# Kernel optimization log

Hardware: AMD Instinct MI355X
Metric: run time of the kernel (lower is better)

## Reference

```python
import jax, jax.numpy as jnp
import numpy as np

CHUNK = 128  # intra-chunk causal block size for the chunked linear-attention scan


def setup_inputs() -> dict:
    key = jax.random.key(0)
    ks = jax.random.split(key, 7)
    B, H, N, D, F = 1, 24, 4096, 128, 256
    q = jax.random.normal(ks[0], (B, H, N, D), dtype=jnp.float32)
    k = jax.random.normal(ks[1], (B, H, N, D), dtype=jnp.float32)
    v = jax.random.normal(ks[2], (B, H, N, D), dtype=jnp.float32)
    # fan-in scaling so phi features / accumulated state stay numerically sane
    w1 = jax.random.normal(ks[3], (F, D), dtype=jnp.float32) * (D ** -0.5)
    b1 = jax.random.normal(ks[4], (F,), dtype=jnp.float32) * 0.02
    w2 = jax.random.normal(ks[5], (F, F), dtype=jnp.float32) * (F ** -0.5)
    b2 = jax.random.normal(ks[6], (F,), dtype=jnp.float32) * 0.02
    return {"q": q, "k": k, "v": v, "w1": w1, "b1": b1, "w2": w2, "b2": b2}


def _phi(x, w1, b1, w2, b2):
    # Linear(D->F) -> SiLU -> Linear(F->F)
    h = jax.nn.silu(jnp.einsum('bnd,fd->bnf', x, w1) + b1)
    return jnp.einsum('bnf,gf->bng', h, w2) + b2


def _causal_scan(qp, kp, vf):
    # out_t = q_t . (sum_{s<=t} k_s v_s^T) / (t+1), chunked parallel form.
    BH, N, F = qp.shape
    D = vf.shape[-1]
    C = CHUNK
    nC = N // C
    qc = qp.reshape(BH, nC, C, F).transpose(1, 0, 2, 3)  # [nC,BH,C,F]
    kc = kp.reshape(BH, nC, C, F).transpose(1, 0, 2, 3)
    vc = vf.reshape(BH, nC, C, D).transpose(1, 0, 2, 3)
    offsets = (jnp.arange(nC) * C).astype(qp.dtype)
    mask = jnp.tril(jnp.ones((C, C), dtype=qp.dtype))  # include diagonal
    pos = jnp.arange(1, C + 1, dtype=qp.dtype)

    def step(w, inp):
        qb, kb, vb, off = inp
        inter = jnp.einsum('bcf,bfd->bcd', qb, w)
        attn = jnp.einsum('bcf,bsf->bcs', qb, kb) * mask
        intra = jnp.einsum('bcs,bsd->bcd', attn, vb)
        counts = off + pos  # global (token_idx + 1)
        out = (inter + intra) / counts[None, :, None]
        w = w + jnp.einsum('bcf,bcd->bfd', kb, vb)
        return w, out

    w0 = jnp.zeros((BH, F, D), dtype=qp.dtype)
    _, outs = jax.lax.scan(step, w0, (qc, kc, vc, offsets))  # outs [nC,BH,C,D]
    return outs.transpose(1, 0, 2, 3).reshape(BH, N, D)


def reference(q, k, v, w1, b1, w2, b2):
    B, H, N, D = q.shape
    qf = q.reshape(B * H, N, D)
    kf = k.reshape(B * H, N, D)
    vf = v.reshape(B * H, N, D)
    qp = _phi(qf, w1, b1, w2, b2)
    kp = _phi(kf, w1, b1, w2, b2)
    out_fwd = _causal_scan(qp, kp, vf)
    out_rev = _causal_scan(qp[:, ::-1], kp[:, ::-1], vf[:, ::-1])[:, ::-1]
    return (out_fwd + out_rev).reshape(B, H, N, D)
```

## Files before the change

### kernel.cpp

```cpp
#include <hip/hip_runtime.h>


typedef __attribute__((ext_vector_type(8))) _Float16 f16x8;
typedef __attribute__((ext_vector_type(4))) _Float16 f16x4;
typedef __attribute__((ext_vector_type(4))) float f32x4;

#define MFMA16(a, b, c) __builtin_amdgcn_mfma_f32_16x16x32_f16((a), (b), (c), 0, 0, 0)

constexpr int BH   = 24;
constexpr int NSEQ = 4096;
constexpr int DD   = 128;
constexpr int FF   = 256;
constexpr int CHK  = 128;
constexpr int NC   = NSEQ / CHK;
constexpr int NROWS = BH * NSEQ;

__global__ void prep_kernel(const float* __restrict__ w1, const float* __restrict__ w2,
                            _Float16* __restrict__ w1h, _Float16* __restrict__ w2h) {
  int i = blockIdx.x * 256 + threadIdx.x;
  if (i < FF * DD) w1h[i] = (_Float16)w1[i];
  if (i < FF * FF) w2h[i] = (_Float16)w2[i];
}

__global__ void vt_kernel(const float* __restrict__ v, _Float16* __restrict__ vT) {
  __shared__ __align__(16) _Float16 lt[128][136];
  int blk = blockIdx.x;
  int c = blk & 31, bh = blk >> 5;
  const float* vc = v + ((size_t)bh * NSEQ + c * CHK) * DD;
  int tid = threadIdx.x;
#pragma unroll
  for (int it = 0; it < 16; ++it) {
    int flat = it * 1024 + tid * 4;
    int s = flat >> 7, d0 = flat & 127;
    float4 xv = *(const float4*)&vc[(size_t)s * DD + d0];
    lt[d0 + 0][s] = (_Float16)xv.x;
    lt[d0 + 1][s] = (_Float16)xv.y;
    lt[d0 + 2][s] = (_Float16)xv.z;
    lt[d0 + 3][s] = (_Float16)xv.w;
  }
  __syncthreads();
#pragma unroll
  for (int it = 0; it < 8; ++it) {
    int flat = it * 256 + tid;
    int d = flat >> 4, sg = flat & 15;
    *(f16x8*)&vT[((size_t)bh * DD + d) * NSEQ + c * CHK + sg * 8] =
        *(const f16x8*)&lt[d][sg * 8];
  }
}

__global__ __launch_bounds__(512, 2)
void phi_kernel(const float* __restrict__ q, const float* __restrict__ k,
                const float* __restrict__ b1, const float* __restrict__ b2,
                const _Float16* __restrict__ w1h, const _Float16* __restrict__ w2h,
                _Float16* __restrict__ qp, _Float16* __restrict__ kp,
                _Float16* __restrict__ kpT) {
  __shared__ __align__(16) char smem[137216];
  _Float16 (*xs)[136]  = (_Float16(*)[136])smem;
  _Float16 (*w1s)[136] = (_Float16(*)[136])(smem + 34816);
  _Float16 (*hs)[264]  = (_Float16(*)[264])smem;
  _Float16 (*w2s)[136] = (_Float16(*)[136])(smem + 67584);
  int blk = blockIdx.x;
  const float* src;
  _Float16* dst;
  bool isk;
  int rb;
  if (blk < NROWS / 128) { src = q; dst = qp; rb = blk * 128; isk = false; }
  else                   { src = k; dst = kp; rb = (blk - NROWS / 128) * 128; isk = true; }
  int tid = threadIdx.x;
  int lane = tid & 63, wv = tid >> 6, lr = lane & 15, lq = lane >> 4;

#pragma unroll
  for (int it = 0; it < 8; ++it) {
    int flat = it * 512 + tid;
    int f = flat >> 4, cg = flat & 15;
    *(f16x8*)&w1s[f][cg * 8] = *(const f16x8*)&w1h[f * DD + cg * 8];
  }
#pragma unroll
  for (int it = 0; it < 8; ++it) {
    int flat = it * 512 + tid;
    int r = flat >> 5, dg = flat & 31;
    float4 xv = *(const float4*)&src[(size_t)(rb + r) * DD + dg * 4];
    f16x4 hv = {(_Float16)xv.x, (_Float16)xv.y, (_Float16)xv.z, (_Float16)xv.w};
    *(f16x4*)&xs[r][dg * 4] = hv;
  }
  __syncthreads();

  int wm1 = wv & 1, wn1 = wv >> 1;
  f32x4 acc[4][4] = {};
#pragma unroll
  for (int ks = 0; ks < 4; ++ks) {
    f16x8 av[4];
#pragma unroll
    for (int im = 0; im < 4; ++im)
      av[im] = *(const f16x8*)&xs[wm1 * 64 + im * 16 + lr][ks * 32 + lq * 8];
#pragma unroll
    for (int fn = 0; fn < 4; ++fn) {
      f16x8 bv = *(const f16x8*)&w1s[wn1 * 64 + fn * 16 + lr][ks * 32 + lq * 8];
#pragma unroll
      for (int im = 0; im < 4; ++im) acc[im][fn] = MFMA16(av[im], bv, acc[im][fn]);
    }
  }
  __syncthreads();

#pragma unroll
  for (int it = 0; it < 8; ++it) {
    int flat = it * 512 + tid;
    int g = flat >> 4, cg = flat & 15;
    *(f16x8*)&w2s[g][cg * 8] = *(const f16x8*)&w2h[(size_t)g * FF + cg * 8];
  }
#pragma unroll
  for (int im = 0; im < 4; ++im)
#pragma unroll
    for (int fn = 0; fn < 4; ++fn) {
      int f = wn1 * 64 + fn * 16 + lr;
      float bb = b1[f];
      int r0 = wm1 * 64 + im * 16 + lq * 4;
#pragma unroll
      for (int r = 0; r < 4; ++r) {
        float xv = acc[im][fn][r] + bb;
        hs[r0 + r][f] = (_Float16)(xv / (1.0f + __expf(-xv)));
      }
    }
  __syncthreads();

  int wmg = wv & 1, wng = wv >> 1;
  f32x4 ac2[4][4] = {};
#pragma unroll
  for (int ks = 0; ks < 4; ++ks) {
    f16x8 av[4];
#pragma unroll
    for (int im = 0; im < 4; ++im)
      av[im] = *(const f16x8*)&hs[wmg * 64 + im * 16 + lr][ks * 32 + lq * 8];
#pragma unroll
    for (int fn = 0; fn < 4; ++fn) {
      f16x8 bv = *(const f16x8*)&w2s[wng * 64 + fn * 16 + lr][ks * 32 + lq * 8];
#pragma unroll
      for (int im = 0; im < 4; ++im) ac2[im][fn] = MFMA16(av[im], bv, ac2[im][fn]);
    }
  }
  __syncthreads();
#pragma unroll
  for (int it = 0; it < 8; ++it) {
    int flat = it * 512 + tid;
    int g = flat >> 4, cg = flat & 15;
    *(f16x8*)&w2s[g][cg * 8] = *(const f16x8*)&w2h[(size_t)g * FF + 128 + cg * 8];
  }
  __syncthreads();
#pragma unroll
  for (int ks = 0; ks < 4; ++ks) {
    f16x8 av[4];
#pragma unroll
    for (int im = 0; im < 4; ++im)
      av[im] = *(const f16x8*)&hs[wmg * 64 + im * 16 + lr][128 + ks * 32 + lq * 8];
#pragma unroll
    for (int fn = 0; fn < 4; ++fn) {
      f16x8 bv = *(const f16x8*)&w2s[wng * 64 + fn * 16 + lr][ks * 32 + lq * 8];
#pragma unroll
      for (int im = 0; im < 4; ++im) ac2[im][fn] = MFMA16(av[im], bv, ac2[im][fn]);
    }
  }

  int bh = rb >> 12, s0 = rb & 4095;
#pragma unroll
  for (int im = 0; im < 4; ++im)
#pragma unroll
    for (int fn = 0; fn < 4; ++fn) {
      int g = wng * 64 + fn * 16 + lr;
      float bb = b2[g];
      int r0 = wmg * 64 + im * 16 + lq * 4;
#pragma unroll
      for (int r = 0; r < 4; ++r) {
        _Float16 val = (_Float16)(ac2[im][fn][r] + bb);
        dst[(size_t)(rb + r0 + r) * FF + g] = val;
        if (isk) kpT[((size_t)bh * FF + g) * NSEQ + s0 + r0 + r] = val;
      }
    }
}

__global__ __launch_bounds__(512, 2)
void s_kernel(const _Float16* __restrict__ vT, const _Float16* __restrict__ kpT,
              _Float16* __restrict__ S) {
  __shared__ __align__(16) _Float16 vt[128][136];
  __shared__ __align__(16) _Float16 kt[256][136];
  int blk = blockIdx.x;
  int c = blk & 31, bh = blk >> 5;
  int tid = threadIdx.x;
#pragma unroll
  for (int it = 0; it < 4; ++it) {
    int flat = it * 512 + tid;
    int d = flat >> 4, sg = flat & 15;
    *(f16x8*)&vt[d][sg * 8] = *(const f16x8*)&vT[((size_t)bh * DD + d) * NSEQ + c * CHK + sg * 8];
  }
#pragma unroll
  for (int it = 0; it < 8; ++it) {
    int flat = it * 512 + tid;
    int f = flat >> 4, sg = flat & 15;
    *(f16x8*)&kt[f][sg * 8] = *(const f16x8*)&kpT[((size_t)bh * FF + f) * NSEQ + c * CHK + sg * 8];
  }
  __syncthreads();
  int lane = tid & 63, wv = tid >> 6, lr = lane & 15, lq = lane >> 4;
  int wmd = wv & 1, wnf = wv >> 1;
  f32x4 acc[4][4] = {};
#pragma unroll
  for (int ks = 0; ks < 4; ++ks) {
    f16x8 av[4];
#pragma unroll
    for (int im = 0; im < 4; ++im)
      av[im] = *(const f16x8*)&vt[wmd * 64 + im * 16 + lr][ks * 32 + lq * 8];
#pragma unroll
    for (int fn = 0; fn < 4; ++fn) {
      f16x8 bv = *(const f16x8*)&kt[wnf * 64 + fn * 16 + lr][ks * 32 + lq * 8];
#pragma unroll
      for (int im = 0; im < 4; ++im) acc[im][fn] = MFMA16(av[im], bv, acc[im][fn]);
    }
  }
  _Float16* Sp = S + ((size_t)bh * NC + c) * (size_t)(DD * FF);
#pragma unroll
  for (int im = 0; im < 4; ++im)
#pragma unroll
    for (int fn = 0; fn < 4; ++fn) {
      int f = wnf * 64 + fn * 16 + lr;
#pragma unroll
      for (int r = 0; r < 4; ++r) {
        int d = wmd * 64 + im * 16 + lq * 4 + r;
        Sp[(size_t)d * FF + f] = (_Float16)acc[im][fn][r];
      }
    }
}

__global__ void prefix_kernel(_Float16* S_Wr, _Float16* __restrict__ Wf) {
  size_t idx = (size_t)blockIdx.x * 256 + threadIdx.x;
  int bh = (int)(idx >> 15);
  int df = (int)(idx & 32767);
  size_t base = (size_t)bh * NC * 32768 + df;
  float vals[NC];
#pragma unroll
  for (int c = 0; c < NC; ++c) vals[c] = (float)S_Wr[base + (size_t)c * 32768];
  float run = 0.f;
#pragma unroll
  for (int c = 0; c < NC; ++c) { Wf[base + (size_t)c * 32768] = (_Float16)run; run += vals[c]; }
  run = 0.f;
#pragma unroll
  for (int c = NC - 1; c >= 0; --c) { S_Wr[base + (size_t)c * 32768] = (_Float16)run; run += vals[c]; }
}

__global__ __launch_bounds__(512, 2)
void scan_kernel(const _Float16* __restrict__ qp, const _Float16* __restrict__ kp,
                 const _Float16* __restrict__ vT, const _Float16* __restrict__ Wf,
                 const _Float16* __restrict__ Wr, float* __restrict__ out) {
  __shared__ __align__(16) _Float16 vt[128][136];
  __shared__ __align__(16) _Float16 P[128][136];
  int blk = blockIdx.x;
  int c = blk & 31, bh = blk >> 5;
  const _Float16* qpc = qp + ((size_t)bh * NSEQ + c * CHK) * FF;
  const _Float16* kpc = kp + ((size_t)bh * NSEQ + c * CHK) * FF;
  int tid = threadIdx.x, lane = tid & 63, wv = tid >> 6, lr = lane & 15, lq = lane >> 4;
  int wm = wv & 3, wn = wv >> 2;

  f16x8 aq[2][8];
#pragma unroll
  for (int im = 0; im < 2; ++im)
#pragma unroll
    for (int ks = 0; ks < 8; ++ks)
      aq[im][ks] = *(const f16x8*)&qpc[(size_t)(wm * 32 + im * 16 + lr) * FF + ks * 32 + lq * 8];
#pragma unroll
  for (int it = 0; it < 4; ++it) {
    int flat = it * 512 + tid;
    int d = flat >> 4, sg = flat & 15;
    *(f16x8*)&vt[d][sg * 8] = *(const f16x8*)&vT[((size_t)bh * DD + d) * NSEQ + c * CHK + sg * 8];
  }
  f16x8 bk[2][8];
#pragma unroll
  for (int ks = 0; ks < 8; ++ks)
    bk[0][ks] = *(const f16x8*)&kpc[(size_t)(wn * 64 + lr) * FF + ks * 32 + lq * 8];
  f32x4 pacc[2][4] = {};
#pragma unroll
  for (int j = 0; j < 4; ++j) {
    int cur = j & 1;
    if (j < 3)
#pragma unroll
      for (int ks = 0; ks < 8; ++ks)
        bk[cur ^ 1][ks] = *(const f16x8*)&kpc[(size_t)(wn * 64 + (j + 1) * 16 + lr) * FF + ks * 32 + lq * 8];
#pragma unroll
    for (int ks = 0; ks < 8; ++ks)
#pragma unroll
      for (int im = 0; im < 2; ++im)
        pacc[im][j] = MFMA16(aq[im][ks], bk[cur][ks], pacc[im][j]);
  }
#pragma unroll
  for (int im = 0; im < 2; ++im)
#pragma unroll
    for (int j = 0; j < 4; ++j)
#pragma unroll
      for (int r = 0; r < 4; ++r)
        P[wm * 32 + im * 16 + lq * 4 + r][wn * 64 + j * 16 + lr] = (_Float16)pacc[im][j][r];

  const _Float16* Wfc = Wf + ((size_t)bh * NC + c) * (size_t)(DD * FF);
  const _Float16* Wrc = Wr + ((size_t)bh * NC + c) * (size_t)(DD * FF);
  f16x8 bf[8], br[8];
#pragma unroll
  for (int ks = 0; ks < 8; ++ks) {
    int d = wn * 64 + lr;
    bf[ks] = *(const f16x8*)&Wfc[(size_t)d * FF + ks * 32 + lq * 8];
    br[ks] = *(const f16x8*)&Wrc[(size_t)d * FF + ks * 32 + lq * 8];
  }
  __syncthreads();

  f32x4 af[2][4] = {}, ar[2][4] = {};
#pragma unroll
  for (int jd = 0; jd < 4; ++jd) {
#pragma unroll
    for (int ks = 0; ks < 8; ++ks)
#pragma unroll
      for (int im = 0; im < 2; ++im) {
        af[im][jd] = MFMA16(aq[im][ks], bf[ks], af[im][jd]);
        ar[im][jd] = MFMA16(aq[im][ks], br[ks], ar[im][jd]);
      }
    if (jd < 3)
#pragma unroll
      for (int ks = 0; ks < 8; ++ks) {
        int d = wn * 64 + (jd + 1) * 16 + lr;
        bf[ks] = *(const f16x8*)&Wfc[(size_t)d * FF + ks * 32 + lq * 8];
        br[ks] = *(const f16x8*)&Wrc[(size_t)d * FF + ks * 32 + lq * 8];
      }
    {
      int ks = jd;
      f16x8 bv[4];
#pragma unroll
      for (int jd2 = 0; jd2 < 4; ++jd2)
        bv[jd2] = *(const f16x8*)&vt[wn * 64 + jd2 * 16 + lr][ks * 32 + lq * 8];
#pragma unroll
      for (int im = 0; im < 2; ++im) {
        int irow = wm * 32 + im * 16 + lr;
        f16x8 p = *(const f16x8*)&P[irow][ks * 32 + lq * 8];
        f16x8 pf = p, pr = p;
#pragma unroll
        for (int jj = 0; jj < 8; ++jj) {
          int s = ks * 32 + lq * 8 + jj;
          pf[jj] = (s <= irow) ? p[jj] : (_Float16)0.0f;
          pr[jj] = (s >= irow) ? p[jj] : (_Float16)0.0f;
        }
#pragma unroll
        for (int jd2 = 0; jd2 < 4; ++jd2) {
          af[im][jd2] = MFMA16(pf, bv[jd2], af[im][jd2]);
          ar[im][jd2] = MFMA16(pr, bv[jd2], ar[im][jd2]);
        }
      }
    }
  }

  float* oc = out + ((size_t)bh * NSEQ + c * CHK) * DD;
#pragma unroll
  for (int im = 0; im < 2; ++im)
#pragma unroll
    for (int jd = 0; jd < 4; ++jd) {
      int d = wn * 64 + jd * 16 + lr;
#pragma unroll
      for (int r = 0; r < 4; ++r) {
        int il = wm * 32 + im * 16 + lq * 4 + r;
        int gi = c * CHK + il;
        oc[(size_t)il * DD + d] = af[im][jd][r] / (float)(gi + 1) + ar[im][jd][r] / (float)(NSEQ - gi);
      }
    }
}

extern "C" void kernel_launch(void* const* d_in, const int* in_sizes, int n_in,
                              void* d_out, int out_size, void* d_ws, size_t ws_size,
                              hipStream_t stream) {
  const float* q  = (const float*)d_in[0];
  const float* k  = (const float*)d_in[1];
  const float* v  = (const float*)d_in[2];
  const float* w1 = (const float*)d_in[3];
  const float* b1 = (const float*)d_in[4];
  const float* w2 = (const float*)d_in[5];
  const float* b2 = (const float*)d_in[6];
  float* out = (float*)d_out;

  char* ws = (char*)d_ws;
  const size_t SZ = 50331648ull;
  _Float16* w1h = (_Float16*)(ws);
  _Float16* w2h = (_Float16*)(ws + 65536);
  _Float16* qp  = (_Float16*)(ws + 196608);
  _Float16* kp  = (_Float16*)(ws + 196608 + SZ);
  _Float16* kpT = (_Float16*)(ws + 196608 + 2 * SZ);
  _Float16* S   = (_Float16*)(ws + 196608 + 3 * SZ);
  _Float16* vT  = (_Float16*)(ws + 196608 + 4 * SZ);
  _Float16* Wf  = kpT;
  _Float16* Wr  = S;

  prep_kernel<<<dim3(256), dim3(256), 0, stream>>>(w1, w2, w1h, w2h);
  vt_kernel<<<dim3(BH * NC), dim3(256), 0, stream>>>(v, vT);
  phi_kernel<<<dim3(2 * NROWS / 128), dim3(512), 0, stream>>>(q, k, b1, b2, w1h, w2h, qp, kp, kpT);
  s_kernel<<<dim3(BH * NC), dim3(512), 0, stream>>>(vT, kpT, S);
  prefix_kernel<<<dim3(BH * DD * FF / 256), dim3(256), 0, stream>>>(S, Wf);
  scan_kernel<<<dim3(BH * NC), dim3(512), 0, stream>>>(qp, kp, vT, Wf, Wr, out);
}
```

Baseline: 416.0 us.

## Shrink phi and S tiles for occupancy, keep weights in registers, vectorize prefix scan

```diff
diff --git a/kernel.cpp b/kernel.cpp
--- a/kernel.cpp
+++ b/kernel.cpp
@@ -48,126 +48,106 @@
   }
 }
 
-__global__ __launch_bounds__(512, 2)
+__global__ __launch_bounds__(512, 4)
 void phi_kernel(const float* __restrict__ q, const float* __restrict__ k,
                 const float* __restrict__ b1, const float* __restrict__ b2,
                 const _Float16* __restrict__ w1h, const _Float16* __restrict__ w2h,
                 _Float16* __restrict__ qp, _Float16* __restrict__ kp,
                 _Float16* __restrict__ kpT) {
-  __shared__ __align__(16) char smem[137216];
-  _Float16 (*xs)[136]  = (_Float16(*)[136])smem;
-  _Float16 (*w1s)[136] = (_Float16(*)[136])(smem + 34816);
-  _Float16 (*hs)[264]  = (_Float16(*)[264])smem;
-  _Float16 (*w2s)[136] = (_Float16(*)[136])(smem + 67584);
+  __shared__ __align__(16) _Float16 xs[64][136];
+  __shared__ __align__(16) _Float16 hs[64][264];
   int blk = blockIdx.x;
   const float* src;
   _Float16* dst;
   bool isk;
   int rb;
-  if (blk < NROWS / 128) { src = q; dst = qp; rb = blk * 128; isk = false; }
-  else                   { src = k; dst = kp; rb = (blk - NROWS / 128) * 128; isk = true; }
+  if (blk < NROWS / 64) { src = q; dst = qp; rb = blk * 64; isk = false; }
+  else                  { src = k; dst = kp; rb = (blk - NROWS / 64) * 64; isk = true; }
   int tid = threadIdx.x;
   int lane = tid & 63, wv = tid >> 6, lr = lane & 15, lq = lane >> 4;
-
-#pragma unroll
-  for (int it = 0; it < 8; ++it) {
-    int flat = it * 512 + tid;
-    int f = flat >> 4, cg = flat & 15;
-    *(f16x8*)&w1s[f][cg * 8] = *(const f16x8*)&w1h[f * DD + cg * 8];
-  }
-#pragma unroll
-  for (int it = 0; it < 8; ++it) {
-    int flat = it * 512 + tid;
-    int r = flat >> 5, dg = flat & 31;
-    float4 xv = *(const float4*)&src[(size_t)(rb + r) * DD + dg * 4];
+  int wn = wv;
+
+  f16x8 w1r[4][2];
+#pragma unroll
+  for (int ks = 0; ks < 4; ++ks)
+#pragma unroll
+    for (int fn = 0; fn < 2; ++fn)
+      w1r[ks][fn] = *(const f16x8*)&w1h[(wn * 32 + fn * 16 + lr) * DD + ks * 32 + lq * 8];
+
+#pragma unroll
+  for (int it = 0; it < 4; ++it) {
+    int flat = it * 2048 + tid * 4;
+    int r = flat >> 7, c = flat & 127;
+    float4 xv = *(const float4*)&src[(size_t)(rb + r) * DD + c];
     f16x4 hv = {(_Float16)xv.x, (_Float16)xv.y, (_Float16)xv.z, (_Float16)xv.w};
-    *(f16x4*)&xs[r][dg * 4] = hv;
-  }
-  __syncthreads();
-
-  int wm1 = wv & 1, wn1 = wv >> 1;
-  f32x4 acc[4][4] = {};
+    *(f16x4*)&xs[r][c] = hv;
+  }
+  __syncthreads();
+
+  f32x4 acc[4][2] = {};
 #pragma unroll
   for (int ks = 0; ks < 4; ++ks) {
     f16x8 av[4];
 #pragma unroll
     for (int im = 0; im < 4; ++im)
-      av[im] = *(const f16x8*)&xs[wm1 * 64 + im * 16 + lr][ks * 32 + lq * 8];
-#pragma unroll
-    for (int fn = 0; fn < 4; ++fn) {
-      f16x8 bv = *(const f16x8*)&w1s[wn1 * 64 + fn * 16 + lr][ks * 32 + lq * 8];
-#pragma unroll
-      for (int im = 0; im < 4; ++im) acc[im][fn] = MFMA16(av[im], bv, acc[im][fn]);
-    }
-  }
-  __syncthreads();
-
-#pragma unroll
-  for (int it = 0; it < 8; ++it) {
-    int flat = it * 512 + tid;
-    int g = flat >> 4, cg = flat & 15;
-    *(f16x8*)&w2s[g][cg * 8] = *(const f16x8*)&w2h[(size_t)g * FF + cg * 8];
-  }
+      av[im] = *(const f16x8*)&xs[im * 16 + lr][ks * 32 + lq * 8];
+#pragma unroll
+    for (int fn = 0; fn < 2; ++fn)
+#pragma unroll
+      for (int im = 0; im < 4; ++im) acc[im][fn] = MFMA16(av[im], w1r[ks][fn], acc[im][fn]);
+  }
+
 #pragma unroll
   for (int im = 0; im < 4; ++im)
 #pragma unroll
-    for (int fn = 0; fn < 4; ++fn) {
-      int f = wn1 * 64 + fn * 16 + lr;
+    for (int fn = 0; fn < 2; ++fn) {
+      int f = wn * 32 + fn * 16 + lr;
       float bb = b1[f];
-      int r0 = wm1 * 64 + im * 16 + lq * 4;
+      int r0 = im * 16 + lq * 4;
 #pragma unroll
       for (int r = 0; r < 4; ++r) {
         float xv = acc[im][fn][r] + bb;
         hs[r0 + r][f] = (_Float16)(xv / (1.0f + __expf(-xv)));
       }
     }
-  __syncthreads();
-
-  int wmg = wv & 1, wng = wv >> 1;
-  f32x4 ac2[4][4] = {};
-#pragma unroll
-  for (int ks = 0; ks < 4; ++ks) {
+
+  f16x8 bw[3][2];
+#pragma unroll
+  for (int fn = 0; fn < 2; ++fn) {
+    int g = wn * 32 + fn * 16 + lr;
+    bw[0][fn] = *(const f16x8*)&w2h[(size_t)g * FF + 0 * 32 + lq * 8];
+    bw[1][fn] = *(const f16x8*)&w2h[(size_t)g * FF + 1 * 32 + lq * 8];
+  }
+  __syncthreads();
+
+  f32x4 ac2[4][2] = {};
+#pragma unroll
+  for (int ks = 0; ks < 8; ++ks) {
+    if (ks < 6) {
+#pragma unroll
+      for (int fn = 0; fn < 2; ++fn) {
+        int g = wn * 32 + fn * 16 + lr;
+        bw[(ks + 2) % 3][fn] = *(const f16x8*)&w2h[(size_t)g * FF + (ks + 2) * 32 + lq * 8];
+      }
+    }
     f16x8 av[4];
 #pragma unroll
     for (int im = 0; im < 4; ++im)
-      av[im] = *(const f16x8*)&hs[wmg * 64 + im * 16 + lr][ks * 32 + lq * 8];
-#pragma unroll
-    for (int fn = 0; fn < 4; ++fn) {
-      f16x8 bv = *(const f16x8*)&w2s[wng * 64 + fn * 16 + lr][ks * 32 + lq * 8];
-#pragma unroll
-      for (int im = 0; im < 4; ++im) ac2[im][fn] = MFMA16(av[im], bv, ac2[im][fn]);
-    }
-  }
-  __syncthreads();
-#pragma unroll
-  for (int it = 0; it < 8; ++it) {
-    int flat = it * 512 + tid;
-    int g = flat >> 4, cg = flat & 15;
-    *(f16x8*)&w2s[g][cg * 8] = *(const f16x8*)&w2h[(size_t)g * FF + 128 + cg * 8];
-  }
-  __syncthreads();
-#pragma unroll
-  for (int ks = 0; ks < 4; ++ks) {
-    f16x8 av[4];
-#pragma unroll
-    for (int im = 0; im < 4; ++im)
-      av[im] = *(const f16x8*)&hs[wmg * 64 + im * 16 + lr][128 + ks * 32 + lq * 8];
-#pragma unroll
-    for (int fn = 0; fn < 4; ++fn) {
-      f16x8 bv = *(const f16x8*)&w2s[wng * 64 + fn * 16 + lr][ks * 32 + lq * 8];
-#pragma unroll
-      for (int im = 0; im < 4; ++im) ac2[im][fn] = MFMA16(av[im], bv, ac2[im][fn]);
-    }
+      av[im] = *(const f16x8*)&hs[im * 16 + lr][ks * 32 + lq * 8];
+#pragma unroll
+    for (int fn = 0; fn < 2; ++fn)
+#pragma unroll
+      for (int im = 0; im < 4; ++im) ac2[im][fn] = MFMA16(av[im], bw[ks % 3][fn], ac2[im][fn]);
   }
 
   int bh = rb >> 12, s0 = rb & 4095;
 #pragma unroll
   for (int im = 0; im < 4; ++im)
 #pragma unroll
-    for (int fn = 0; fn < 4; ++fn) {
-      int g = wng * 64 + fn * 16 + lr;
+    for (int fn = 0; fn < 2; ++fn) {
+      int g = wn * 32 + fn * 16 + lr;
       float bb = b2[g];
-      int r0 = wmg * 64 + im * 16 + lq * 4;
+      int r0 = im * 16 + lq * 4;
 #pragma unroll
       for (int r = 0; r < 4; ++r) {
         _Float16 val = (_Float16)(ac2[im][fn][r] + bb);
@@ -177,13 +157,13 @@
     }
 }
 
-__global__ __launch_bounds__(512, 2)
+__global__ __launch_bounds__(512, 4)
 void s_kernel(const _Float16* __restrict__ vT, const _Float16* __restrict__ kpT,
               _Float16* __restrict__ S) {
   __shared__ __align__(16) _Float16 vt[128][136];
-  __shared__ __align__(16) _Float16 kt[256][136];
+  __shared__ __align__(16) _Float16 kt[128][136];
   int blk = blockIdx.x;
-  int c = blk & 31, bh = blk >> 5;
+  int fh = blk & 1, c = (blk >> 1) & 31, bh = blk >> 6;
   int tid = threadIdx.x;
 #pragma unroll
   for (int it = 0; it < 4; ++it) {
@@ -192,15 +172,16 @@
     *(f16x8*)&vt[d][sg * 8] = *(const f16x8*)&vT[((size_t)bh * DD + d) * NSEQ + c * CHK + sg * 8];
   }
 #pragma unroll
-  for (int it = 0; it < 8; ++it) {
+  for (int it = 0; it < 4; ++it) {
     int flat = it * 512 + tid;
     int f = flat >> 4, sg = flat & 15;
-    *(f16x8*)&kt[f][sg * 8] = *(const f16x8*)&kpT[((size_t)bh * FF + f) * NSEQ + c * CHK + sg * 8];
+    *(f16x8*)&kt[f][sg * 8] =
+        *(const f16x8*)&kpT[((size_t)bh * FF + fh * 128 + f) * NSEQ + c * CHK + sg * 8];
   }
   __syncthreads();
   int lane = tid & 63, wv = tid >> 6, lr = lane & 15, lq = lane >> 4;
   int wmd = wv & 1, wnf = wv >> 1;
-  f32x4 acc[4][4] = {};
+  f32x4 acc[4][2] = {};
 #pragma unroll
   for (int ks = 0; ks < 4; ++ks) {
     f16x8 av[4];
@@ -208,8 +189,8 @@
     for (int im = 0; im < 4; ++im)
       av[im] = *(const f16x8*)&vt[wmd * 64 + im * 16 + lr][ks * 32 + lq * 8];
 #pragma unroll
-    for (int fn = 0; fn < 4; ++fn) {
-      f16x8 bv = *(const f16x8*)&kt[wnf * 64 + fn * 16 + lr][ks * 32 + lq * 8];
+    for (int fn = 0; fn < 2; ++fn) {
+      f16x8 bv = *(const f16x8*)&kt[wnf * 32 + fn * 16 + lr][ks * 32 + lq * 8];
 #pragma unroll
       for (int im = 0; im < 4; ++im) acc[im][fn] = MFMA16(av[im], bv, acc[im][fn]);
     }
@@ -218,8 +199,8 @@
 #pragma unroll
   for (int im = 0; im < 4; ++im)
 #pragma unroll
-    for (int fn = 0; fn < 4; ++fn) {
-      int f = wnf * 64 + fn * 16 + lr;
+    for (int fn = 0; fn < 2; ++fn) {
+      int f = fh * 128 + wnf * 32 + fn * 16 + lr;
 #pragma unroll
       for (int r = 0; r < 4; ++r) {
         int d = wmd * 64 + im * 16 + lq * 4 + r;
@@ -229,19 +210,30 @@
 }
 
 __global__ void prefix_kernel(_Float16* S_Wr, _Float16* __restrict__ Wf) {
-  size_t idx = (size_t)blockIdx.x * 256 + threadIdx.x;
-  int bh = (int)(idx >> 15);
-  int df = (int)(idx & 32767);
-  size_t base = (size_t)bh * NC * 32768 + df;
-  float vals[NC];
-#pragma unroll
-  for (int c = 0; c < NC; ++c) vals[c] = (float)S_Wr[base + (size_t)c * 32768];
-  float run = 0.f;
-#pragma unroll
-  for (int c = 0; c < NC; ++c) { Wf[base + (size_t)c * 32768] = (_Float16)run; run += vals[c]; }
-  run = 0.f;
-#pragma unroll
-  for (int c = NC - 1; c >= 0; --c) { S_Wr[base + (size_t)c * 32768] = (_Float16)run; run += vals[c]; }
+  size_t t8 = (size_t)blockIdx.x * 256 + threadIdx.x;
+  int bh = (int)(t8 >> 12);
+  int df8 = (int)(t8 & 4095);
+  size_t base = (size_t)bh * NC * 32768 + (size_t)df8 * 8;
+  f16x8 vals[NC];
+#pragma unroll
+  for (int c = 0; c < NC; ++c) vals[c] = *(const f16x8*)&S_Wr[base + (size_t)c * 32768];
+  float run[8] = {};
+#pragma unroll
+  for (int c = 0; c < NC; ++c) {
+    f16x8 w;
+#pragma unroll
+    for (int j = 0; j < 8; ++j) { w[j] = (_Float16)run[j]; run[j] += (float)vals[c][j]; }
+    *(f16x8*)&Wf[base + (size_t)c * 32768] = w;
+  }
+#pragma unroll
+  for (int j = 0; j < 8; ++j) run[j] = 0.f;
+#pragma unroll
+  for (int c = NC - 1; c >= 0; --c) {
+    f16x8 w;
+#pragma unroll
+    for (int j = 0; j < 8; ++j) { w[j] = (_Float16)run[j]; run[j] += (float)vals[c][j]; }
+    *(f16x8*)&S_Wr[base + (size_t)c * 32768] = w;
+  }
 }
 
 __global__ __launch_bounds__(512, 2)
@@ -390,8 +382,8 @@
 
   prep_kernel<<<dim3(256), dim3(256), 0, stream>>>(w1, w2, w1h, w2h);
   vt_kernel<<<dim3(BH * NC), dim3(256), 0, stream>>>(v, vT);
-  phi_kernel<<<dim3(2 * NROWS / 128), dim3(512), 0, stream>>>(q, k, b1, b2, w1h, w2h, qp, kp, kpT);
-  s_kernel<<<dim3(BH * NC), dim3(512), 0, stream>>>(vT, kpT, S);
-  prefix_kernel<<<dim3(BH * DD * FF / 256), dim3(256), 0, stream>>>(S, Wf);
+  phi_kernel<<<dim3(2 * NROWS / 64), dim3(512), 0, stream>>>(q, k, b1, b2, w1h, w2h, qp, kp, kpT);
+  s_kernel<<<dim3(BH * NC * 2), dim3(512), 0, stream>>>(vT, kpT, S);
+  prefix_kernel<<<dim3(BH * 4096 / 256), dim3(256), 0, stream>>>(S, Wf);
   scan_kernel<<<dim3(BH * NC), dim3(512), 0, stream>>>(qp, kp, vT, Wf, Wr, out);
 }
```

Measured after the change: 458.0 us. 1.1x slower.
